# Kernel optimization log

Measured on AMD Instinct MI355X. Metric: run time of the kernel, lower is better.

The kernel has to match this reference:

```python
import jax, jax.numpy as jnp
import numpy as np
from jax import lax

L = 128       # layers_num (sequential recurrence length)
D = 262144    # input_dim


def setup_inputs() -> dict:
    key = jax.random.key(0)
    ks = jax.random.split(key, 7)
    x = jax.random.normal(ks[0], (L, D), dtype=jnp.float32)
    weight_x = jax.random.normal(ks[1], (L, D), dtype=jnp.float32) * 0.1 + 1.0
    weight_g = jax.random.normal(ks[2], (L, D), dtype=jnp.float32) * 0.1 + 1.0
    weight_u = jax.random.normal(ks[3], (L, D), dtype=jnp.float32) * 0.1 + 1.0
    mask = jax.random.uniform(ks[4], (L, D), dtype=jnp.float32)
    fc_w = jax.random.normal(ks[5], (1, D), dtype=jnp.float32) * (1.0 / np.sqrt(D))
    fc_b = jax.random.normal(ks[6], (1,), dtype=jnp.float32) * 0.01
    return {"x": x, "weight_x": weight_x, "weight_g": weight_g,
            "weight_u": weight_u, "mask": mask, "fc_w": fc_w, "fc_b": fc_b}


def reference(x, weight_x, weight_g, weight_u, mask, fc_w, fc_b):
    sg = lax.stop_gradient
    # t = 0 initialization (mirrors the .detach() calls in the torch code)
    xbar0 = sg(x[0])                              # x_bar[0]
    h0 = jnp.tanh(sg(x[0]) * weight_x[0])         # h[0]
    xbar1 = sg(h0) * weight_g[0] + x[0]           # x_bar[1]

    def step(carry, inp):
        h_prev, xbar_t = carry                    # h[t-1], x_bar[t], each [D]
        xt, mt, wxt, wut, wgt = inp
        x_trans = xt * mt + xbar_t * (1.0 - mt)
        u = jnp.tanh(x_trans * wxt)
        f = jax.nn.sigmoid(sg(h_prev) + u * wut) * mt
        h_t = f * h_prev + (1.0 - f) * u
        h_t = h0 + jax.nn.relu(h_t - h0)
        xbar_next = sg(h_t) * wgt + sg(x_trans)   # x_bar[t+1]
        return (h_t, xbar_next), xbar_t

    xs = (x[1:], mask[1:], weight_x[1:], weight_u[1:], weight_g[1:])
    _, xbar_seq = lax.scan(step, (h0, xbar1), xs)  # x_bar[1..L-1], [L-1, D]
    x_bar = jnp.concatenate([xbar0[None], xbar_seq], axis=0)  # [L, D]
    pred = jax.nn.sigmoid(x_bar @ fc_w.T + fc_b)   # [L, 1]
    return pred
```

## Files before the change

kernel.cpp:

```cpp
#include <hip/hip_runtime.h>


#define L     128
#define DCOLS 262144
#define TPB   256
#define NWAVE (TPB / 64)
#define NBLK  (DCOLS / TPB)

__device__ __forceinline__ float wred(float v) {
#pragma unroll
    for (int o = 32; o > 0; o >>= 1) v += __shfl_xor(v, o, 64);
    return v;
}

__device__ __forceinline__ float rcpf(float x) { return __builtin_amdgcn_rcpf(x); }

__device__ __forceinline__ float ftanh(float a) {
    a = fminf(fmaxf(a, -15.f), 15.f);
    float e = __expf(-2.f * a);
    return (1.f - e) * rcpf(1.f + e);
}

__device__ __forceinline__ float fsig(float z) {
    return rcpf(1.f + __expf(-z));
}

__global__ __launch_bounds__(TPB) void rnn_main(
    const float* __restrict__ x,  const float* __restrict__ wx,
    const float* __restrict__ wg, const float* __restrict__ wu,
    const float* __restrict__ m,  const float* __restrict__ fcw,
    float* __restrict__ part)
{
    __shared__ float lacc[NWAVE][L];
    const int tid  = threadIdx.x;
    const int lane = tid & 63;
    const int wid  = tid >> 6;
    const int col  = blockIdx.x * TPB + tid;

    const float* px  = x  + col;
    const float* pm  = m  + col;
    const float* pwx = wx + col;
    const float* pwu = wu + col;
    const float* pwg = wg + col;

    const float fw = fcw[col];

    float x0  = px[0];
    float wx0 = pwx[0];
    float wg0 = pwg[0];

    float h0 = ftanh(x0 * wx0);
    float h  = h0;
    float xb = h0 * wg0 + x0;

    {
        float s = wred(x0 * fw);
        if (lane == 0) lacc[wid][0] = s;
    }

    float Ax = px[DCOLS],  Am = pm[DCOLS],  Awx = pwx[DCOLS],
          Awu = pwu[DCOLS], Awg = pwg[DCOLS];
    float Bx = px[2*DCOLS], Bm = pm[2*DCOLS], Bwx = pwx[2*DCOLS],
          Bwu = pwu[2*DCOLS], Bwg = pwg[2*DCOLS];

#define STEP(T, XR, MR, WXR, WUR, WGR)                                   \
    {                                                                    \
        float s = wred(xb * fw);                      \
        if (lane == 0) lacc[wid][(T)] = s;                               \
        float xt = (XR) * (MR) + xb * (1.f - (MR));                      \
        float u  = ftanh(xt * (WXR));                                    \
        float f  = fsig(h + u * (WUR)) * (MR);                           \
        float hn = f * h + (1.f - f) * u;                                \
        h  = fmaxf(hn, h0);                         \
        xb = h * (WGR) + xt;                                             \
    }

    int t = 1;
    for (; t + 1 < L; t += 2) {
        {
            float xc = Ax, mc = Am, wxc = Awx, wuc = Awu, wgc = Awg;
            if (t + 2 < L) {
                const long o = (long)(t + 2) * DCOLS;
                Ax = px[o]; Am = pm[o]; Awx = pwx[o]; Awu = pwu[o]; Awg = pwg[o];
            }
            STEP(t, xc, mc, wxc, wuc, wgc);
        }
        {
            float xc = Bx, mc = Bm, wxc = Bwx, wuc = Bwu, wgc = Bwg;
            if (t + 3 < L) {
                const long o = (long)(t + 3) * DCOLS;
                Bx = px[o]; Bm = pm[o]; Bwx = pwx[o]; Bwu = pwu[o]; Bwg = pwg[o];
            }
            STEP(t + 1, xc, mc, wxc, wuc, wgc);
        }
    }
    STEP(t, Ax, Am, Awx, Awu, Awg);
#undef STEP

    __syncthreads();
    if (tid < L) {
        float s = 0.f;
#pragma unroll
        for (int w = 0; w < NWAVE; ++w) s += lacc[w][tid];
        part[blockIdx.x * L + tid] = s;
    }
}

__global__ __launch_bounds__(64) void rnn_finish(
    const float* __restrict__ part, const float* __restrict__ fcb,
    float* __restrict__ out)
{
    const int t    = blockIdx.x;
    const int lane = threadIdx.x;
    float s = 0.f;
    for (int b = lane; b < NBLK; b += 64) s += part[b * L + t];
    s = wred(s);
    if (lane == 0) out[t] = fsig(s + fcb[0]);
}

extern "C" void kernel_launch(void* const* d_in, const int* in_sizes, int n_in,
                              void* d_out, int out_size, void* d_ws, size_t ws_size,
                              hipStream_t stream) {
    const float* x   = (const float*)d_in[0];
    const float* wx  = (const float*)d_in[1];
    const float* wg  = (const float*)d_in[2];
    const float* wu  = (const float*)d_in[3];
    const float* m   = (const float*)d_in[4];
    const float* fcw = (const float*)d_in[5];
    const float* fcb = (const float*)d_in[6];
    float* out  = (float*)d_out;
    float* part = (float*)d_ws;

    rnn_main<<<NBLK, TPB, 0, stream>>>(x, wx, wg, wu, m, fcw, part);
    rnn_finish<<<L, 64, 0, stream>>>(part, fcb, out);
}
```

Before: 121.7 us.

## Process four columns per thread with float4 loads and LDS-tiled reduction

Each thread now owns four adjacent columns and loads them as float4, in single-wave blocks with a 4-deep register prefetch pipeline instead of 2-deep. The per-step 64-lane shuffle reduction is replaced by writing per-lane dot products into a 16x68 LDS tile and flushing every 16 timesteps with one transposed reduction. Tanh and the gate update are rewritten with fewer operations. The aim is to cut shuffle and reduction overhead per timestep and raise memory-level parallelism, at the cost of far fewer threads in flight (1024 waves total) and more registers per thread.

```diff
diff --git a/kernel.cpp b/kernel.cpp
--- a/kernel.cpp
+++ b/kernel.cpp
@@ -3,107 +3,121 @@
 
 #define L     128
 #define DCOLS 262144
-#define TPB   256
-#define NWAVE (TPB / 64)
-#define NBLK  (DCOLS / TPB)
-
-__device__ __forceinline__ float wred(float v) {
-#pragma unroll
-    for (int o = 32; o > 0; o >>= 1) v += __shfl_xor(v, o, 64);
-    return v;
-}
+#define TPB   64
+#define NBLK  (DCOLS / (4 * TPB))
+#define RS    (DCOLS / 4)
 
 __device__ __forceinline__ float rcpf(float x) { return __builtin_amdgcn_rcpf(x); }
 
 __device__ __forceinline__ float ftanh(float a) {
-    a = fminf(fmaxf(a, -15.f), 15.f);
+    a = fmaxf(a, -15.f);
     float e = __expf(-2.f * a);
-    return (1.f - e) * rcpf(1.f + e);
+    float r = rcpf(1.f + e);
+    return 2.f * r - 1.f;
 }
 
 __device__ __forceinline__ float fsig(float z) {
     return rcpf(1.f + __expf(-z));
 }
 
-__global__ __launch_bounds__(TPB) void rnn_main(
+__device__ __forceinline__ void upd1(float& h, float& xb, float h0,
+                                     float xc, float mc, float wxc,
+                                     float wuc, float wgc) {
+    float xt = xb + mc * (xc - xb);
+    float u  = ftanh(xt * wxc);
+    float f  = fsig(h + u * wuc) * mc;
+    h  = fmaxf(u + f * (h - u), h0);
+    xb = h * wgc + xt;
+}
+
+__global__ __launch_bounds__(TPB, 1) void rnn_main(
     const float* __restrict__ x,  const float* __restrict__ wx,
     const float* __restrict__ wg, const float* __restrict__ wu,
     const float* __restrict__ m,  const float* __restrict__ fcw,
     float* __restrict__ part)
 {
-    __shared__ float lacc[NWAVE][L];
-    const int tid  = threadIdx.x;
-    const int lane = tid & 63;
-    const int wid  = tid >> 6;
-    const int col  = blockIdx.x * TPB + tid;
+    __shared__ float tile[16][68];
+    const int lane = threadIdx.x;
+    const int col4 = blockIdx.x * TPB + lane;
 
-    const float* px  = x  + col;
-    const float* pm  = m  + col;
-    const float* pwx = wx + col;
-    const float* pwu = wu + col;
-    const float* pwg = wg + col;
+    const float4* px  = (const float4*)x  + col4;
+    const float4* pm  = (const float4*)m  + col4;
+    const float4* pwx = (const float4*)wx + col4;
+    const float4* pwu = (const float4*)wu + col4;
+    const float4* pwg = (const float4*)wg + col4;
+    const float4 fw = ((const float4*)fcw)[col4];
 
-    const float fw = fcw[col];
+    float4 x0 = px[0], wx0 = pwx[0], wg0 = pwg[0];
+    float4 h0, h, xb;
+    h0.x = ftanh(x0.x * wx0.x); h0.y = ftanh(x0.y * wx0.y);
+    h0.z = ftanh(x0.z * wx0.z); h0.w = ftanh(x0.w * wx0.w);
+    h = h0;
+    xb.x = h0.x * wg0.x + x0.x; xb.y = h0.y * wg0.y + x0.y;
+    xb.z = h0.z * wg0.z + x0.z; xb.w = h0.w * wg0.w + x0.w;
 
-    float x0  = px[0];
-    float wx0 = pwx[0];
-    float wg0 = pwg[0];
+    tile[0][lane] = x0.x*fw.x + x0.y*fw.y + x0.z*fw.z + x0.w*fw.w;
 
-    float h0 = ftanh(x0 * wx0);
-    float h  = h0;
-    float xb = h0 * wg0 + x0;
-
-    {
-        float s = wred(x0 * fw);
-        if (lane == 0) lacc[wid][0] = s;
+#define FLUSH(TBASE)                                                        \
+    {                                                                       \
+        const float4* rp =                                                  \
+            (const float4*)(&tile[lane & 15][0] + ((lane >> 4) * 16));      \
+        float4 a0 = rp[0], a1 = rp[1], a2 = rp[2], a3 = rp[3];              \
+        float p = ((a0.x + a0.y) + (a0.z + a0.w))                           \
+                + ((a1.x + a1.y) + (a1.z + a1.w))                           \
+                + ((a2.x + a2.y) + (a2.z + a2.w))                           \
+                + ((a3.x + a3.y) + (a3.z + a3.w));                          \
+        p += __shfl_xor(p, 16, 64);                                         \
+        p += __shfl_xor(p, 32, 64);                                         \
+        if (lane < 16) part[blockIdx.x * L + (TBASE) + lane] = p;           \
     }
 
-    float Ax = px[DCOLS],  Am = pm[DCOLS],  Awx = pwx[DCOLS],
-          Awu = pwu[DCOLS], Awg = pwg[DCOLS];
-    float Bx = px[2*DCOLS], Bm = pm[2*DCOLS], Bwx = pwx[2*DCOLS],
-          Bwu = pwu[2*DCOLS], Bwg = pwg[2*DCOLS];
-
-#define STEP(T, XR, MR, WXR, WUR, WGR)                                   \
-    {                                                                    \
-        float s = wred(xb * fw);                      \
-        if (lane == 0) lacc[wid][(T)] = s;                               \
-        float xt = (XR) * (MR) + xb * (1.f - (MR));                      \
-        float u  = ftanh(xt * (WXR));                                    \
-        float f  = fsig(h + u * (WUR)) * (MR);                           \
-        float hn = f * h + (1.f - f) * u;                                \
-        h  = fmaxf(hn, h0);                         \
-        xb = h * (WGR) + xt;                                             \
+#define STEP(T, BX, BM, BWX, BWU, BWG)                                      \
+    {                                                                       \
+        tile[(T) & 15][lane] =                                              \
+            xb.x*fw.x + xb.y*fw.y + xb.z*fw.z + xb.w*fw.w;                  \
+        upd1(h.x, xb.x, h0.x, BX.x, BM.x, BWX.x, BWU.x, BWG.x);             \
+        upd1(h.y, xb.y, h0.y, BX.y, BM.y, BWX.y, BWU.y, BWG.y);             \
+        upd1(h.z, xb.z, h0.z, BX.z, BM.z, BWX.z, BWU.z, BWG.z);             \
+        upd1(h.w, xb.w, h0.w, BX.w, BM.w, BWX.w, BWU.w, BWG.w);             \
+        if (((T) & 15) == 15) FLUSH((T) - 15);                              \
     }
 
-    int t = 1;
-    for (; t + 1 < L; t += 2) {
+    float4 Ax = px[1*RS], Am = pm[1*RS], Awx = pwx[1*RS], Awu = pwu[1*RS], Awg = pwg[1*RS];
+    float4 Bx = px[2*RS], Bm = pm[2*RS], Bwx = pwx[2*RS], Bwu = pwu[2*RS], Bwg = pwg[2*RS];
+    float4 Cx = px[3*RS], Cm = pm[3*RS], Cwx = pwx[3*RS], Cwu = pwu[3*RS], Cwg = pwg[3*RS];
+    float4 Dx = px[4*RS], Dm = pm[4*RS], Dwx = pwx[4*RS], Dwu = pwu[4*RS], Dwg = pwg[4*RS];
+
+    for (int t = 1; t < 122; t += 4) {
         {
-            float xc = Ax, mc = Am, wxc = Awx, wuc = Awu, wgc = Awg;
-            if (t + 2 < L) {
-                const long o = (long)(t + 2) * DCOLS;
-                Ax = px[o]; Am = pm[o]; Awx = pwx[o]; Awu = pwu[o]; Awg = pwg[o];
-            }
-            STEP(t, xc, mc, wxc, wuc, wgc);
+            float4 cx = Ax, cm = Am, cwx = Awx, cwu = Awu, cwg = Awg;
+            long o = (long)((t + 4 > 127) ? 127 : t + 4) * RS;
+            Ax = px[o]; Am = pm[o]; Awx = pwx[o]; Awu = pwu[o]; Awg = pwg[o];
+            STEP(t, cx, cm, cwx, cwu, cwg);
         }
         {
-            float xc = Bx, mc = Bm, wxc = Bwx, wuc = Bwu, wgc = Bwg;
-            if (t + 3 < L) {
-                const long o = (long)(t + 3) * DCOLS;
-                Bx = px[o]; Bm = pm[o]; Bwx = pwx[o]; Bwu = pwu[o]; Bwg = pwg[o];
-            }
-            STEP(t + 1, xc, mc, wxc, wuc, wgc);
+            float4 cx = Bx, cm = Bm, cwx = Bwx, cwu = Bwu, cwg = Bwg;
+            long o = (long)((t + 5 > 127) ? 127 : t + 5) * RS;
+            Bx = px[o]; Bm = pm[o]; Bwx = pwx[o]; Bwu = pwu[o]; Bwg = pwg[o];
+            STEP(t + 1, cx, cm, cwx, cwu, cwg);
+        }
+        {
+            float4 cx = Cx, cm = Cm, cwx = Cwx, cwu = Cwu, cwg = Cwg;
+            long o = (long)((t + 6 > 127) ? 127 : t + 6) * RS;
+            Cx = px[o]; Cm = pm[o]; Cwx = pwx[o]; Cwu = pwu[o]; Cwg = pwg[o];
+            STEP(t + 2, cx, cm, cwx, cwu, cwg);
+        }
+        {
+            float4 cx = Dx, cm = Dm, cwx = Dwx, cwu = Dwu, cwg = Dwg;
+            long o = (long)((t + 7 > 127) ? 127 : t + 7) * RS;
+            Dx = px[o]; Dm = pm[o]; Dwx = pwx[o]; Dwu = pwu[o]; Dwg = pwg[o];
+            STEP(t + 3, cx, cm, cwx, cwu, cwg);
         }
     }
-    STEP(t, Ax, Am, Awx, Awu, Awg);
+    STEP(125, Ax, Am, Awx, Awu, Awg);
+    STEP(126, Bx, Bm, Bwx, Bwu, Bwg);
+    STEP(127, Cx, Cm, Cwx, Cwu, Cwg);
 #undef STEP
-
-    __syncthreads();
-    if (tid < L) {
-        float s = 0.f;
-#pragma unroll
-        for (int w = 0; w < NWAVE; ++w) s += lacc[w][tid];
-        part[blockIdx.x * L + tid] = s;
-    }
+#undef FLUSH
 }
 
 __global__ __launch_bounds__(64) void rnn_finish(
@@ -113,8 +127,10 @@
     const int t    = blockIdx.x;
     const int lane = threadIdx.x;
     float s = 0.f;
-    for (int b = lane; b < NBLK; b += 64) s += part[b * L + t];
-    s = wred(s);
+#pragma unroll
+    for (int i = 0; i < NBLK / 64; ++i) s += part[(i * 64 + lane) * L + t];
+#pragma unroll
+    for (int o = 32; o > 0; o >>= 1) s += __shfl_xor(s, o, 64);
     if (lane == 0) out[t] = fsig(s + fcb[0]);
 }
 
```

Result: no change. 122.2 us (+0.4%).
